# Kernel optimization log

Measured on AMD Instinct MI355X. Metric: run time of the kernel, lower is better.

Reference implementation:

```python
import jax, jax.numpy as jnp
import numpy as np

HEADS = 8
NUM_LANDMARKS = 256
PINV_ITERS = 6
KERNEL = 33
PAD = KERNEL // 2


def moore_penrose_iter_pinv(x, iters=PINV_ITERS):
    abs_x = jnp.abs(x)
    col = abs_x.sum(axis=-1)
    row = abs_x.sum(axis=-2)
    z = jnp.swapaxes(x, -1, -2) / (jnp.max(col) * jnp.max(row))
    I = jnp.eye(x.shape[-1], dtype=x.dtype)
    for _ in range(iters):
        xz = x @ z
        z = 0.25 * z @ (13.0 * I - xz @ (15.0 * I - xz @ (7.0 * I - xz)))
    return z


def setup_inputs() -> dict:
    key = jax.random.key(0)
    k1, k2, k3, k4 = jax.random.split(key, 4)
    b, h, n, d = 2, HEADS, 8192, 64
    q = jax.random.normal(k1, (b, h, n, d), dtype=jnp.float32)
    k = jax.random.normal(k2, (b, h, n, d), dtype=jnp.float32)
    v = jax.random.normal(k3, (b, h, n, d), dtype=jnp.float32)
    conv_w = jax.random.normal(k4, (HEADS, 1, KERNEL, 1), dtype=jnp.float32) * 0.05
    return {"q": q, "k": k, "v": v, "conv_w": conv_w}


def reference(q, k, v, conv_w):
    b, h, n, d = q.shape
    m = NUM_LANDMARKS
    l = n // m  # n chosen divisible by m, so no padding branch

    # landmarks: mean over contiguous groups of size l
    q_land = q.reshape(b, h, m, l, d).sum(axis=-2) / l  # [b,h,m,d]
    k_land = k.reshape(b, h, m, l, d).sum(axis=-2) / l

    sim1 = jnp.einsum('bhid,bhjd->bhij', q, k_land)       # [b,h,n,m]
    sim2 = jnp.einsum('bhid,bhjd->bhij', q_land, k_land)  # [b,h,m,m]
    sim3 = jnp.einsum('bhid,bhjd->bhij', q_land, k)       # [b,h,m,n]

    attn1 = jax.nn.softmax(sim1, axis=-1)
    attn2 = jax.nn.softmax(sim2, axis=-1)
    attn3 = jax.nn.softmax(sim3, axis=-1)

    attn2_inv = moore_penrose_iter_pinv(attn2, PINV_ITERS)

    out = attn1 @ (attn2_inv @ (attn3 @ v))  # [b,h,n,d]

    # depthwise residual conv over sequence dim (Conv2d(h,h,(33,1),groups=h,bias=False) on v)
    res = jax.lax.conv_general_dilated(
        v, conv_w,
        window_strides=(1, 1),
        padding=((PAD, PAD), (0, 0)),
        dimension_numbers=('NCHW', 'OIHW', 'NCHW'),
        feature_group_count=HEADS,
    )
    return out + res
```

## Files before the change

### kernel.cpp

```cpp
#include <hip/hip_runtime.h>


#define N_SEQ 8192
#define NBH   16
#define MLAND 256
#define DHEAD 64
#define NSPLIT3 8
#define MM_E  (NBH * MLAND * MLAND)
#define LM_E  (NBH * MLAND * DHEAD)

typedef __attribute__((ext_vector_type(8))) short bfrag;
typedef __attribute__((ext_vector_type(8))) _Float16 hfrag;
typedef __attribute__((ext_vector_type(4))) float f32x4;

__device__ __forceinline__ void fma8(float (&o)[8], float p, const float4& a, const float4& b) {
    o[0] += p * a.x; o[1] += p * a.y; o[2] += p * a.z; o[3] += p * a.w;
    o[4] += p * b.x; o[5] += p * b.y; o[6] += p * b.z; o[7] += p * b.w;
}

__device__ __forceinline__ float bf2f(unsigned short h) {
    return __uint_as_float(((unsigned)h) << 16);
}

__device__ __forceinline__ void splitbf(float v, unsigned short& h, unsigned short& l) {
    unsigned bits = __float_as_uint(v);
    h = (unsigned short)(bits >> 16);
    float r = v - __uint_as_float(bits & 0xffff0000u);
    l = (unsigned short)(__float_as_uint(r) >> 16);
}

__device__ __forceinline__ void splith(float v, unsigned short& h, unsigned short& l) {
    _Float16 hf = (_Float16)v;
    _Float16 lf = (_Float16)(v - (float)hf);
    h = __builtin_bit_cast(unsigned short, hf);
    l = __builtin_bit_cast(unsigned short, lf);
}

__device__ __forceinline__ void stage16(const float* __restrict__ src,
                                        unsigned short* dh, unsigned short* dl) {
    unsigned* ph = (unsigned*)dh;
    unsigned* pl = (unsigned*)dl;
    #pragma unroll
    for (int o = 0; o < 16; o += 4) {
        float4 a = *(const float4*)(src + o);
        float vv[4] = {a.x, a.y, a.z, a.w};
        unsigned short h[4], l[4];
        #pragma unroll
        for (int u = 0; u < 4; ++u) splitbf(vv[u], h[u], l[u]);
        ph[o / 2]     = (unsigned)h[0] | ((unsigned)h[1] << 16);
        ph[o / 2 + 1] = (unsigned)h[2] | ((unsigned)h[3] << 16);
        pl[o / 2]     = (unsigned)l[0] | ((unsigned)l[1] << 16);
        pl[o / 2 + 1] = (unsigned)l[2] | ((unsigned)l[3] << 16);
    }
}

__device__ __forceinline__ void stageh16(const float* __restrict__ src,
                                         unsigned short* dh, unsigned short* dl) {
    unsigned* ph = (unsigned*)dh;
    unsigned* pl = (unsigned*)dl;
    #pragma unroll
    for (int o = 0; o < 16; o += 4) {
        float4 a = *(const float4*)(src + o);
        float vv[4] = {a.x, a.y, a.z, a.w};
        unsigned short h[4], l[4];
        #pragma unroll
        for (int u = 0; u < 4; ++u) splith(vv[u], h[u], l[u]);
        ph[o / 2]     = (unsigned)h[0] | ((unsigned)h[1] << 16);
        ph[o / 2 + 1] = (unsigned)h[2] | ((unsigned)h[3] << 16);
        pl[o / 2]     = (unsigned)l[0] | ((unsigned)l[1] << 16);
        pl[o / 2 + 1] = (unsigned)l[2] | ((unsigned)l[3] << 16);
    }
}

__global__ __launch_bounds__(64) void k_landmarks(
    const float* __restrict__ q, const float* __restrict__ k,
    float* __restrict__ ql, float* __restrict__ kl)
{
    int mi = blockIdx.x & 255;
    int bh = blockIdx.x >> 8;
    const float* src = blockIdx.y ? k : q;
    float*       dst = blockIdx.y ? kl : ql;
    int t = threadIdx.x;
    const float* s = src + ((size_t)bh * N_SEQ + (size_t)mi * 32) * DHEAD;
    float acc = 0.f;
    #pragma unroll
    for (int j = 0; j < 32; ++j) acc += s[j * DHEAD + t];
    dst[((size_t)bh * MLAND + mi) * DHEAD + t] = acc * (1.f / 32.f);
}

__global__ __launch_bounds__(256) void k_sim2_softmax(
    const float* __restrict__ ql, const float* __restrict__ kl,
    unsigned short* __restrict__ xs)
{
    unsigned short* xh = xs;
    unsigned short* xl = xs + MM_E;
    int bh = blockIdx.x >> 8;
    int i  = blockIdx.x & 255;
    int t  = threadIdx.x;
    __shared__ float qrow[DHEAD];
    __shared__ float wred[8];
    if (t < DHEAD) qrow[t] = ql[((size_t)bh * MLAND + i) * DHEAD + t];
    __syncthreads();
    const float* krow = kl + ((size_t)bh * MLAND + t) * DHEAD;
    float s = 0.f;
    #pragma unroll
    for (int kk = 0; kk < DHEAD; kk += 4) {
        float4 k4 = *(const float4*)(krow + kk);
        s += qrow[kk] * k4.x + qrow[kk + 1] * k4.y + qrow[kk + 2] * k4.z + qrow[kk + 3] * k4.w;
    }
    float m = s;
    #pragma unroll
    for (int o = 32; o > 0; o >>= 1) m = fmaxf(m, __shfl_xor(m, o, 64));
    int wave = t >> 6, lane = t & 63;
    if (lane == 0) wred[wave] = m;
    __syncthreads();
    float bm = fmaxf(fmaxf(wred[0], wred[1]), fmaxf(wred[2], wred[3]));
    float e = __expf(s - bm);
    float sum = e;
    #pragma unroll
    for (int o = 32; o > 0; o >>= 1) sum += __shfl_xor(sum, o, 64);
    if (lane == 0) wred[4 + wave] = sum;
    __syncthreads();
    float bs = wred[4] + wred[5] + wred[6] + wred[7];
    float val = e / bs;
    unsigned short h, l;
    splitbf(val, h, l);
    size_t idx = ((size_t)bh * MLAND + i) * MLAND + t;
    xh[idx] = h;
    xl[idx] = l;
}

__global__ __launch_bounds__(256) void k_scale_reduce(
    const unsigned short* __restrict__ xs, float* __restrict__ scl)
{
    const unsigned short* xh = xs;
    const unsigned short* xl = xs + MM_E;
    int bh = blockIdx.y, seg = blockIdx.x;
    int t = threadIdx.x;
    size_t b = (size_t)bh * MLAND * MLAND;
    __shared__ float red[32];
    __shared__ float red2[256];

    {
        int r = seg * 16 + (t >> 4);
        int j0 = (t & 15) * 16;
        float rp = 0.f;
        #pragma unroll
        for (int j = 0; j < 16; ++j) {
            size_t idx = b + (size_t)r * MLAND + j0 + j;
            rp += bf2f(xh[idx]) + bf2f(xl[idx]);
        }
        rp += __shfl_xor(rp, 1, 16);
        rp += __shfl_xor(rp, 2, 16);
        rp += __shfl_xor(rp, 4, 16);
        rp += __shfl_xor(rp, 8, 16);
        if ((t & 15) == 0) red[t >> 4] = rp;
        __syncthreads();
        if (t == 0) {
            float m = red[0];
            #pragma unroll
            for (int i = 1; i < 16; ++i) m = fmaxf(m, red[i]);
            atomicMax((unsigned int*)&scl[0], __float_as_uint(m));
        }
        __syncthreads();
    }
    {
        int c = seg * 16 + (t & 15);
        int i0 = (t >> 4) * 16;
        float cp = 0.f;
        #pragma unroll
        for (int i = 0; i < 16; ++i) {
            size_t idx = b + (size_t)(i0 + i) * MLAND + c;
            cp += bf2f(xh[idx]) + bf2f(xl[idx]);
        }
        red2[t] = cp;
        __syncthreads();
        if (t < 16) {
            float s = 0.f;
            #pragma unroll
            for (int g = 0; g < 16; ++g) s += red2[g * 16 + t];
            red[t] = s;
        }
        __syncthreads();
        if (t == 0) {
            float m = red[0];
            #pragma unroll
            for (int i = 1; i < 16; ++i) m = fmaxf(m, red[i]);
            atomicMax((unsigned int*)&scl[1], __float_as_uint(m));
        }
    }
}

__global__ __launch_bounds__(256) void k_zinit(
    const unsigned short* __restrict__ xs, unsigned short* __restrict__ zs,
    const float* __restrict__ scl)
{
    const unsigned short* xh = xs;
    const unsigned short* xl = xs + MM_E;
    unsigned short* zh = zs;
    unsigned short* zl = zs + MM_E;
    __shared__ float tile[32][33];
    int bh = blockIdx.z;
    int i0 = blockIdx.y * 32, j0 = blockIdx.x * 32;
    int t = threadIdx.x;
    int lx = t & 31, ly = t >> 5;
    size_t b = (size_t)bh * MLAND * MLAND;
    #pragma unroll
    for (int p = 0; p < 4; ++p) {
        size_t idx = b + (size_t)(i0 + ly + 8 * p) * MLAND + j0 + lx;
        tile[ly + 8 * p][lx] = bf2f(xh[idx]) + bf2f(xl[idx]);
    }
    __syncthreads();
    float inv = 1.0f / (scl[0] * scl[1]);
    #pragma unroll
    for (int p = 0; p < 4; ++p) {
        float val = tile[lx][ly + 8 * p] * inv;
        unsigned short h, l;
        splitbf(val, h, l);
        size_t idx = b + (size_t)(j0 + ly + 8 * p) * MLAND + i0 + lx;
        zh[idx] = h;
        zl[idx] = l;
    }
}

__global__ __launch_bounds__(256) void k_bmm_planes(
    const unsigned short* __restrict__ Ahp, const unsigned short* __restrict__ Alp,
    const unsigned short* __restrict__ Bhp, const unsigned short* __restrict__ Blp,
    unsigned short* __restrict__ Chp, unsigned short* __restrict__ Clp,
    float* __restrict__ Cf,
    int N, float diag, float bscale, float outscale)
{
    __shared__ unsigned short sm[2 * 32 * 72 + 2 * 64 * 72];
    unsigned short* Ah = sm;
    unsigned short* Al = sm + 32 * 72;
    unsigned short* Bh = sm + 2 * 32 * 72;
    unsigned short* Bl = sm + 2 * 32 * 72 + 64 * 72;

    int ntn = N >> 6;
    int bid = blockIdx.x;
    int xcd  = bid & 7;
    int slot = bid >> 3;
    int bh   = xcd + 8 * (slot & 1);
    int tile = slot >> 1;
    int m0 = (tile / ntn) * 32, n0 = (tile % ntn) * 64;

    const size_t abase = (size_t)bh * 65536;
    const size_t bbase = (size_t)bh * 256 * N;
    int t = threadIdx.x;
    int wave = t >> 6, lane = t & 63;
    int l15 = lane & 15, quad = lane >> 4;
    int wr = wave >> 1, wc = wave & 1;
    unsigned sflip = (bscale < 0.f) ? 0x8000u : 0u;

    f32x4 acc[2] = {};

    for (int kc = 0; kc < 256; kc += 64) {
        __syncthreads();
        {
            int m = t & 31, ks = (t >> 5) * 8;
            size_t off = abase + (size_t)(m0 + m) * 256 + kc + ks;
            *(uint4*)&Ah[m * 72 + ks] = *(const uint4*)&Ahp[off];
            *(uint4*)&Al[m * 72 + ks] = *(const uint4*)&Alp[off];
        }
        {
            int kk = t & 63, ns = (t >> 6) * 16;
            int gk = kc + kk;
            size_t off = bbase + (size_t)gk * N + n0 + ns;
            unsigned short hb[16], lb[16];
            *(uint4*)&hb[0] = *(const uint4*)&Bhp[off];
            *(uint4*)&hb[8] = *(const uint4*)&Bhp[off + 8];
            *(uint4*)&lb[0] = *(const uint4*)&Blp[off];
            *(uint4*)&lb[8] = *(const uint4*)&Blp[off + 8];
            #pragma unroll
            for (int u = 0; u < 16; ++u) {
                unsigned short h = hb[u] ^ sflip;
                unsigned short l = lb[u] ^ sflip;
                if (diag != 0.f && gk == n0 + ns + u) {
                    float val = diag + bf2f(h) + bf2f(l);
                    splitbf(val, h, l);
                }
                Bh[(ns + u) * 72 + kk] = h;
                Bl[(ns + u) * 72 + kk] = l;
            }
        }
        __syncthreads();

        #pragma unroll
        for (int k0 = 0; k0 < 64; k0 += 32) {
            int kf = k0 + quad * 8;
            int am = wr * 16 + l15;
            bfrag ah = *(const bfrag*)&Ah[am * 72 + kf];
            bfrag al = *(const bfrag*)&Al[am * 72 + kf];
            #pragma unroll
            for (int j = 0; j < 2; ++j) {
                int bn = wc * 32 + j * 16 + l15;
                bfrag bhf = *(const bfrag*)&Bh[bn * 72 + kf];
                bfrag blf = *(const bfrag*)&Bl[bn * 72 + kf];
                acc[j] = __builtin_amdgcn_mfma_f32_16x16x32_bf16(al, bhf, acc[j], 0, 0, 0);
                acc[j] = __builtin_amdgcn_mfma_f32_16x16x32_bf16(ah, blf, acc[j], 0, 0, 0);
                acc[j] = __builtin_amdgcn_mfma_f32_16x16x32_bf16(ah, bhf, acc[j], 0, 0, 0);
            }
        }
    }

    size_t cbase = (size_t)bh * 256 * N;
    if (Cf) {
        #pragma unroll
        for (int j = 0; j < 2; ++j) {
            #pragma unroll
            for (int r = 0; r < 4; ++r) {
                int row = m0 + wr * 16 + quad * 4 + r;
                int col = n0 + wc * 32 + j * 16 + l15;
                Cf[cbase + (size_t)row * N + col] = acc[j][r] * outscale;
            }
        }
    } else {
        #pragma unroll
        for (int j = 0; j < 2; ++j) {
            #pragma unroll
            for (int r = 0; r < 4; ++r) {
                int row = m0 + wr * 16 + quad * 4 + r;
                int col = n0 + wc * 32 + j * 16 + l15;
                float val = acc[j][r] * outscale;
                unsigned short h, l;
                splitbf(val, h, l);
                size_t idx = cbase + (size_t)row * N + col;
                Chp[idx] = h;
                Clp[idx] = l;
            }
        }
    }
}

__global__ __launch_bounds__(256, 2) void k_attn3_partial(
    const float* __restrict__ ql, const float* __restrict__ k,
    const float* __restrict__ v, float* __restrict__ pO,
    float* __restrict__ pm, float* __restrict__ pl)
{
    __shared__ __align__(16) unsigned short sm3[36864];
    unsigned short* QH = sm3;
    unsigned short* QL = sm3 + 4608;
    unsigned short* KH = sm3 + 9216;
    unsigned short* KL = sm3 + 13824;
    unsigned short* VH = sm3 + 18432;
    unsigned short* VL = sm3 + 23040;
    unsigned short* PH = sm3 + 27648;
    unsigned short* PL = sm3 + 32256;

    int sp = blockIdx.x;
    int m0 = blockIdx.y * 64;
    int bh = blockIdx.z;
    int t = threadIdx.x;
    int wave = t >> 6, lane = t & 63;
    int l15 = lane & 15, quad = lane >> 4;

    {
        int row = t & 63, ds = (t >> 6) * 16;
        const float* src = ql + ((size_t)bh * MLAND + m0 + row) * DHEAD + ds;
        stage16(src, &QH[row * 72 + ds], &QL[row * 72 + ds]);
    }
    __syncthreads();

    bfrag aqh[2], aql[2];
    #pragma unroll
    for (int ks = 0; ks < 2; ++ks) {
        aqh[ks] = *(const bfrag*)&QH[(wave * 16 + l15) * 72 + ks * 32 + quad * 8];
        aql[ks] = *(const bfrag*)&QL[(wave * 16 + l15) * 72 + ks * 32 + quad * 8];
    }

    f32x4 O[4] = {};
    float M[4], L[4];
    #pragma unroll
    for (int r = 0; r < 4; ++r) { M[r] = -1e30f; L[r] = 0.f; }

    const float* kb = k + (size_t)bh * N_SEQ * DHEAD;
    const float* vb = v + (size_t)bh * N_SEQ * DHEAD;

    for (int cc = 0; cc < 16; ++cc) {
        int c0 = sp * 1024 + cc * 64;
        __syncthreads();
        {
            int key = t & 63, ds = (t >> 6) * 16;
            stage16(kb + (size_t)(c0 + key) * DHEAD + ds,
                    &KH[key * 72 + ds], &KL[key * 72 + ds]);
        }
        {
            int key = t & 63, dq = (t >> 6) * 16;
            const float* src = vb + (size_t)(c0 + key) * DHEAD + dq;
            #pragma unroll
            for (int o = 0; o < 16; o += 4) {
                float4 a = *(const float4*)(src + o);
                float vv[4] = {a.x, a.y, a.z, a.w};
                #pragma unroll
                for (int u = 0; u < 4; ++u) {
                    unsigned short h, l;
                    splitbf(vv[u], h, l);
                    VH[(dq + o + u) * 72 + key] = h;
                    VL[(dq + o + u) * 72 + key] = l;
                }
            }
        }
        __syncthreads();

        f32x4 S4[4] = {};
        __builtin_amdgcn_s_setprio(1);
        #pragma unroll
        for (int ks = 0; ks < 2; ++ks) {
            #pragma unroll
            for (int ni = 0; ni < 4; ++ni) {
                bfrag bkh = *(const bfrag*)&KH[(ni * 16 + l15) * 72 + ks * 32 + quad * 8];
                bfrag bkl = *(const bfrag*)&KL[(ni * 16 + l15) * 72 + ks * 32 + quad * 8];
                S4[ni] = __builtin_amdgcn_mfma_f32_16x16x32_bf16(aql[ks], bkh, S4[ni], 0, 0, 0);
                S4[ni] = __builtin_amdgcn_mfma_f32_16x16x32_bf16(aqh[ks], bkl, S4[ni], 0, 0, 0);
                S4[ni] = __builtin_amdgcn_mfma_f32_16x16x32_bf16(aqh[ks], bkh, S4[ni], 0, 0, 0);
            }
        }
        __builtin_amdgcn_s_setprio(0);

        #pragma unroll
        for (int r = 0; r < 4; ++r) {
            float mv = fmaxf(fmaxf(S4[0][r], S4[1][r]), fmaxf(S4[2][r], S4[3][r]));
            mv = fmaxf(mv, __shfl_xor(mv, 1, 16));
            mv = fmaxf(mv, __shfl_xor(mv, 2, 16));
            mv = fmaxf(mv, __shfl_xor(mv, 4, 16));
            mv = fmaxf(mv, __shfl_xor(mv, 8, 16));
            float nM = fmaxf(M[r], mv);
            float alpha = __expf(M[r] - nM);
            M[r] = nM;
            float rs = 0.f;
            #pragma unroll
            for (int ni = 0; ni < 4; ++ni) {
                float p = __expf(S4[ni][r] - nM);
                S4[ni][r] = p;
                rs += p;
            }
            rs += __shfl_xor(rs, 1, 16);
            rs += __shfl_xor(rs, 2, 16);
            rs += __shfl_xor(rs, 4, 16);
            rs += __shfl_xor(rs, 8, 16);
            L[r] = L[r] * alpha + rs;
            #pragma unroll
            for (int ni = 0; ni < 4; ++ni) O[ni][r] *= alpha;
        }

        #pragma unroll
        for (int ni = 0; ni < 4; ++ni) {
            #pragma unroll
            for (int r = 0; r < 4; ++r) {
                int row = wave * 16 + quad * 4 + r;
                int col = ni * 16 + l15;
                unsigned short h, l;
                splitbf(S4[ni][r], h, l);
                PH[row * 72 + col] = h;
                PL[row * 72 + col] = l;
            }
        }

        __builtin_amdgcn_s_setprio(1);
        #pragma unroll
        for (int ks = 0; ks < 2; ++ks) {
            bfrag aph = *(const bfrag*)&PH[(wave * 16 + l15) * 72 + ks * 32 + quad * 8];
            bfrag apl = *(const bfrag*)&PL[(wave * 16 + l15) * 72 + ks * 32 + quad * 8];
            #pragma unroll
            for (int ni = 0; ni < 4; ++ni) {
                bfrag bvh = *(const bfrag*)&VH[(ni * 16 + l15) * 72 + ks * 32 + quad * 8];
                bfrag bvl = *(const bfrag*)&VL[(ni * 16 + l15) * 72 + ks * 32 + quad * 8];
                O[ni] = __builtin_amdgcn_mfma_f32_16x16x32_bf16(apl, bvh, O[ni], 0, 0, 0);
                O[ni] = __builtin_amdgcn_mfma_f32_16x16x32_bf16(aph, bvl, O[ni], 0, 0, 0);
                O[ni] = __builtin_amdgcn_mfma_f32_16x16x32_bf16(aph, bvh, O[ni], 0, 0, 0);
            }
        }
        __builtin_amdgcn_s_setprio(0);
    }

    int base = (bh * NSPLIT3 + sp) * MLAND + m0;
    #pragma unroll
    for (int r = 0; r < 4; ++r) {
        int row = wave * 16 + quad * 4 + r;
        if (l15 == 0) { pm[base + row] = M[r]; pl[base + row] = L[r]; }
        #pragma unroll
        for (int ni = 0; ni < 4; ++ni)
            pO[(size_t)(base + row) * DHEAD + ni * 16 + l15] = O[ni][r];
    }
}

__global__ __launch_bounds__(64) void k_attn3_combine(
    const float* __restrict__ pO, const float* __restrict__ pm,
    const float* __restrict__ pl, unsigned short* __restrict__ kvs)
{
    unsigned short* kvh = kvs;
    unsigned short* kvl = kvs + LM_E;
    int bh = blockIdx.x >> 8;
    int m  = blockIdx.x & 255;
    int d  = threadIdx.x;
    float M = -1e30f;
    #pragma unroll
    for (int s = 0; s < NSPLIT3; ++s) M = fmaxf(M, pm[(bh * NSPLIT3 + s) * MLAND + m]);
    float L = 0.f, O = 0.f;
    #pragma unroll
    for (int s = 0; s < NSPLIT3; ++s) {
        int base = (bh * NSPLIT3 + s) * MLAND + m;
        float w = __expf(pm[base] - M);
        L += pl[base] * w;
        O += w * pO[(size_t)base * DHEAD + d];
    }
    float val = O / L;
    unsigned short h, l;
    splitbf(val, h, l);
    size_t idx = ((size_t)bh * MLAND + m) * DHEAD + d;
    kvh[idx] = h;
    kvl[idx] = l;
}

__global__ __launch_bounds__(256, 2) void k_attn1_mfma(
    const float* __restrict__ q, const float* __restrict__ kl,
    const float* __restrict__ W, float* __restrict__ out)
{
    __shared__ __align__(16) unsigned short sm1[36864];
    unsigned short* QH = sm1;
    unsigned short* QL = sm1 + 4608;
    unsigned short* KH = sm1 + 9216;
    unsigned short* KL = sm1 + 13824;
    unsigned short* WH = sm1 + 18432;
    unsigned short* WL = sm1 + 23040;
    unsigned short* PH = sm1 + 27648;
    unsigned short* PL = sm1 + 32256;

    int bh = blockIdx.y;
    int r0 = blockIdx.x * 64;
    int t = threadIdx.x;
    int wave = t >> 6, lane = t & 63;
    int l15 = lane & 15, quad = lane >> 4;

    {
        int row = t & 63, ds = (t >> 6) * 16;
        const float* src = q + ((size_t)bh * N_SEQ + r0 + row) * DHEAD + ds;
        stageh16(src, &QH[row * 72 + ds], &QL[row * 72 + ds]);
    }
    __syncthreads();

    hfrag aqh[2], aql[2];
    #pragma unroll
    for (int ks = 0; ks < 2; ++ks) {
        aqh[ks] = *(const hfrag*)&QH[(wave * 16 + l15) * 72 + ks * 32 + quad * 8];
        aql[ks] = *(const hfrag*)&QL[(wave * 16 + l15) * 72 + ks * 32 + quad * 8];
    }

    f32x4 O4[4] = {};
    float M[4], L[4];
    #pragma unroll
    for (int r = 0; r < 4; ++r) { M[r] = -1e30f; L[r] = 0.f; }

    for (int mc = 0; mc < 4; ++mc) {
        __syncthreads();
        {
            int key = t & 63, ds = (t >> 6) * 16;
            stageh16(kl + ((size_t)bh * MLAND + mc * 64 + key) * DHEAD + ds,
                     &KH[key * 72 + ds], &KL[key * 72 + ds]);
        }
        {
            int key = t & 63, dq = (t >> 6) * 16;
            const float* src = W + ((size_t)bh * MLAND + mc * 64 + key) * DHEAD + dq;
            #pragma unroll
            for (int o = 0; o < 16; o += 4) {
                float4 a = *(const float4*)(src + o);
                float vv[4] = {a.x * 0.015625f, a.y * 0.015625f,
                               a.z * 0.015625f, a.w * 0.015625f};
                #pragma unroll
                for (int u = 0; u < 4; ++u) {
                    unsigned short h, l;
                    splith(vv[u], h, l);
                    WH[(dq + o + u) * 72 + key] = h;
                    WL[(dq + o + u) * 72 + key] = l;
                }
            }
        }
        __syncthreads();

        f32x4 S4[4] = {};
        __builtin_amdgcn_s_setprio(1);
        #pragma unroll
        for (int ks = 0; ks < 2; ++ks) {
            #pragma unroll
            for (int ni = 0; ni < 4; ++ni) {
                hfrag bkh = *(const hfrag*)&KH[(ni * 16 + l15) * 72 + ks * 32 + quad * 8];
                hfrag bkl = *(const hfrag*)&KL[(ni * 16 + l15) * 72 + ks * 32 + quad * 8];
                S4[ni] = __builtin_amdgcn_mfma_f32_16x16x32_f16(aql[ks], bkh, S4[ni], 0, 0, 0);
                S4[ni] = __builtin_amdgcn_mfma_f32_16x16x32_f16(aqh[ks], bkl, S4[ni], 0, 0, 0);
                S4[ni] = __builtin_amdgcn_mfma_f32_16x16x32_f16(aqh[ks], bkh, S4[ni], 0, 0, 0);
            }
        }
        __builtin_amdgcn_s_setprio(0);

        #pragma unroll
        for (int r = 0; r < 4; ++r) {
            float mv = fmaxf(fmaxf(S4[0][r], S4[1][r]), fmaxf(S4[2][r], S4[3][r]));
            mv = fmaxf(mv, __shfl_xor(mv, 1, 16));
            mv = fmaxf(mv, __shfl_xor(mv, 2, 16));
            mv = fmaxf(mv, __shfl_xor(mv, 4, 16));
            mv = fmaxf(mv, __shfl_xor(mv, 8, 16));
            float nM = fmaxf(M[r], mv);
            float alpha = __expf(M[r] - nM);
            M[r] = nM;
            float rs = 0.f;
            #pragma unroll
            for (int ni = 0; ni < 4; ++ni) {
                float p = __expf(S4[ni][r] - nM);
                S4[ni][r] = p;
                rs += p;
            }
            rs += __shfl_xor(rs, 1, 16);
            rs += __shfl_xor(rs, 2, 16);
            rs += __shfl_xor(rs, 4, 16);
            rs += __shfl_xor(rs, 8, 16);
            L[r] = L[r] * alpha + rs;
            #pragma unroll
            for (int ni = 0; ni < 4; ++ni) O4[ni][r] *= alpha;
        }

        #pragma unroll
        for (int ni = 0; ni < 4; ++ni) {
            #pragma unroll
            for (int r = 0; r < 4; ++r) {
                int row = wave * 16 + quad * 4 + r;
                int col = ni * 16 + l15;
                unsigned short h, l;
                splith(S4[ni][r], h, l);
                PH[row * 72 + col] = h;
                PL[row * 72 + col] = l;
            }
        }

        __builtin_amdgcn_s_setprio(1);
        #pragma unroll
        for (int ks = 0; ks < 2; ++ks) {
            hfrag aph = *(const hfrag*)&PH[(wave * 16 + l15) * 72 + ks * 32 + quad * 8];
            hfrag apl = *(const hfrag*)&PL[(wave * 16 + l15) * 72 + ks * 32 + quad * 8];
            #pragma unroll
            for (int ni = 0; ni < 4; ++ni) {
                hfrag bwh = *(const hfrag*)&WH[(ni * 16 + l15) * 72 + ks * 32 + quad * 8];
                hfrag bwl = *(const hfrag*)&WL[(ni * 16 + l15) * 72 + ks * 32 + quad * 8];
                O4[ni] = __builtin_amdgcn_mfma_f32_16x16x32_f16(apl, bwh, O4[ni], 0, 0, 0);
                O4[ni] = __builtin_amdgcn_mfma_f32_16x16x32_f16(aph, bwl, O4[ni], 0, 0, 0);
                O4[ni] = __builtin_amdgcn_mfma_f32_16x16x32_f16(aph, bwh, O4[ni], 0, 0, 0);
            }
        }
        __builtin_amdgcn_s_setprio(0);
    }

    float inv[4];
    #pragma unroll
    for (int r = 0; r < 4; ++r) inv[r] = 64.0f / L[r];
    #pragma unroll
    for (int r = 0; r < 4; ++r) {
        int row = wave * 16 + quad * 4 + r;
        float* dst = out + ((size_t)bh * N_SEQ + r0 + row) * DHEAD;
        #pragma unroll
        for (int ni = 0; ni < 4; ++ni)
            dst[ni * 16 + l15] = O4[ni][r] * inv[r];
    }
}

__global__ __launch_bounds__(256) void k_conv_add(
    const float* __restrict__ v, const float* __restrict__ cw,
    float* __restrict__ out)
{
    __shared__ __align__(16) float smem[160 * 68];
    __shared__ float wgt[33];
    int bh = blockIdx.y;
    int r0 = blockIdx.x * 128;
    int t = threadIdx.x;
    int wave = t >> 6, lane = t & 63;
    int ly = lane >> 3, lx = lane & 7;
    int rb = wave * 32 + ly * 4;

    if (t < 33) wgt[t] = cw[(bh & 7) * 33 + t];

    for (int rr = t; rr < 160; rr += 256) {
        int gr = r0 - 16 + rr;
        bool ok = (gr >= 0) && (gr < N_SEQ);
        const float* src = v + ((size_t)bh * N_SEQ + gr) * DHEAD;
        #pragma unroll
        for (int c = 0; c < 64; c += 4) {
            float4 val = ok ? *(const float4*)(src + c) : make_float4(0.f, 0.f, 0.f, 0.f);
            *(float4*)&smem[rr * 68 + c] = val;
        }
    }
    __syncthreads();

    float res[4][8] = {};
    #pragma unroll
    for (int w = 0; w < 36; ++w) {
        float4 va  = *(const float4*)&smem[(rb + w) * 68 + lx * 8];
        float4 vb4 = *(const float4*)&smem[(rb + w) * 68 + lx * 8 + 4];
        #pragma unroll
        for (int i = 0; i < 4; ++i) {
            if (w - i >= 0 && w - i <= 32) {
                float wv = wgt[w - i];
                fma8(res[i], wv, va, vb4);
            }
        }
    }

    #pragma unroll
    for (int i = 0; i < 4; ++i) {
        float* dst = out + ((size_t)bh * N_SEQ + r0 + rb + i) * DHEAD + lx * 8;
        float4 o0 = *(const float4*)dst;
        float4 o1 = *(const float4*)(dst + 4);
        *(float4*)dst = make_float4(o0.x + res[i][0], o0.y + res[i][1],
                                    o0.z + res[i][2], o0.w + res[i][3]);
        *(float4*)(dst + 4) = make_float4(o1.x + res[i][4], o1.y + res[i][5],
                                          o1.z + res[i][6], o1.w + res[i][7]);
    }
}

extern "C" void kernel_launch(void* const* d_in, const int* in_sizes, int n_in,
                              void* d_out, int out_size, void* d_ws, size_t ws_size,
                              hipStream_t stream)
{
    (void)in_sizes; (void)n_in; (void)out_size; (void)ws_size;
    const float* q  = (const float*)d_in[0];
    const float* k  = (const float*)d_in[1];
    const float* v  = (const float*)d_in[2];
    const float* cw = (const float*)d_in[3];
    float* out = (float*)d_out;
    float* ws  = (float*)d_ws;

    const size_t LM = (size_t)LM_E;
    const size_t MM = (size_t)MM_E;

    float* ql  = ws;
    float* kl  = ql  + LM;
    float* xsf = kl  + LM;
    float* zsf = xsf + MM;
    float* big = zsf + MM;
    float* kvf = big + 4 * MM;
    float* W   = kvf + LM;
    float* scl = W   + LM;
    float* pm  = scl + 16;
    float* pl  = pm + (size_t)NBH * NSPLIT3 * MLAND;

    float* pO = big;

    unsigned short* xs  = (unsigned short*)xsf;
    unsigned short* zs  = (unsigned short*)zsf;
    unsigned short* bgu = (unsigned short*)big;
    unsigned short* kvs = (unsigned short*)kvf;

    unsigned short* xh  = xs;
    unsigned short* xl  = xs + MM;
    unsigned short* zh  = zs;
    unsigned short* zl  = zs + MM;
    unsigned short* z2h = bgu;
    unsigned short* z2l = bgu + MM;
    unsigned short* xzh = bgu + 2 * MM;
    unsigned short* xzl = bgu + 3 * MM;
    unsigned short* t2h = bgu + 4 * MM;
    unsigned short* t2l = bgu + 5 * MM;
    unsigned short* t3h = bgu + 6 * MM;
    unsigned short* t3l = bgu + 7 * MM;
    unsigned short* kvh = kvs;
    unsigned short* kvl = kvs + LM;

    hipMemsetAsync(scl, 0, 32, stream);

    k_landmarks<<<dim3(NBH * MLAND, 2), 64, 0, stream>>>(q, k, ql, kl);
    k_sim2_softmax<<<NBH * MLAND, 256, 0, stream>>>(ql, kl, xs);
    k_scale_reduce<<<dim3(16, NBH), 256, 0, stream>>>(xs, scl);
    k_zinit<<<dim3(8, 8, NBH), 256, 0, stream>>>(xs, zs, scl);

    k_attn3_partial<<<dim3(NSPLIT3, 4, NBH), 256, 0, stream>>>(ql, k, v, pO, pm, pl);
    k_attn3_combine<<<NBH * MLAND, 64, 0, stream>>>(pO, pm, pl, kvs);

    unsigned short *zch = zh, *zcl = zl, *znh = z2h, *znl = z2l;
    for (int it = 0; it < 6; ++it) {
        k_bmm_planes<<<512, 256, 0, stream>>>(
            xh, xl, zch, zcl, xzh, xzl, nullptr, 256, 0.f, 1.f, 1.f);
        k_bmm_planes<<<512, 256, 0, stream>>>(
            xzh, xzl, xzh, xzl, t2h, t2l, nullptr, 256, 7.f, -1.f, 1.f);
        k_bmm_planes<<<512, 256, 0, stream>>>(
            xzh, xzl, t2h, t2l, t3h, t3l, nullptr, 256, 15.f, -1.f, 1.f);
        k_bmm_planes<<<512, 256, 0, stream>>>(
            zch, zcl, t3h, t3l, znh, znl, nullptr, 256, 13.f, -1.f, 0.25f);
        unsigned short* th = zch; zch = znh; znh = th;
        unsigned short* tl = zcl; zcl = znl; znl = tl;
    }
    k_bmm_planes<<<128, 256, 0, stream>>>(
        zch, zcl, kvh, kvl, nullptr, nullptr, W, 64, 0.f, 1.f, 1.f);

    k_attn1_mfma<<<dim3(128, NBH), 256, 0, stream>>>(q, kl, W, out);
    k_conv_add<<<dim3(64, NBH), 256, 0, stream>>>(v, cw, out);
}
```

Baseline: 568.1 us.

## Widen k-chunk to 128 and prefetch second half into registers in bmm_planes

Replaces the four-iteration k-loop (64-wide chunks) in the split-bf16 batched matmul with two 128-wide chunks. The global loads for the second chunk are issued into registers before the first chunk's MFMAs run, overlapping memory latency with compute and halving the number of barrier pairs. The shared-memory footprint roughly doubles and register pressure grows, which may reduce occupancy.

```diff
diff --git a/kernel.cpp b/kernel.cpp
--- a/kernel.cpp
+++ b/kernel.cpp
@@ -230,11 +230,11 @@
     float* __restrict__ Cf,
     int N, float diag, float bscale, float outscale)
 {
-    __shared__ unsigned short sm[2 * 32 * 72 + 2 * 64 * 72];
+    __shared__ __align__(16) unsigned short sm[26112];
     unsigned short* Ah = sm;
-    unsigned short* Al = sm + 32 * 72;
-    unsigned short* Bh = sm + 2 * 32 * 72;
-    unsigned short* Bl = sm + 2 * 32 * 72 + 64 * 72;
+    unsigned short* Al = sm + 4352;
+    unsigned short* Bh = sm + 8704;
+    unsigned short* Bl = sm + 17408;
 
     int ntn = N >> 6;
     int bid = blockIdx.x;
@@ -252,54 +252,110 @@
     int wr = wave >> 1, wc = wave & 1;
     unsigned sflip = (bscale < 0.f) ? 0x8000u : 0u;
 
+    int am_ = t & 31, aks = (t >> 5) * 16;
+    int bkk = t & 127, bns = (t >> 7) * 32;
+
     f32x4 acc[2] = {};
-
-    for (int kc = 0; kc < 256; kc += 64) {
-        __syncthreads();
-        {
-            int m = t & 31, ks = (t >> 5) * 8;
-            size_t off = abase + (size_t)(m0 + m) * 256 + kc + ks;
-            *(uint4*)&Ah[m * 72 + ks] = *(const uint4*)&Ahp[off];
-            *(uint4*)&Al[m * 72 + ks] = *(const uint4*)&Alp[off];
-        }
-        {
-            int kk = t & 63, ns = (t >> 6) * 16;
-            int gk = kc + kk;
-            size_t off = bbase + (size_t)gk * N + n0 + ns;
-            unsigned short hb[16], lb[16];
-            *(uint4*)&hb[0] = *(const uint4*)&Bhp[off];
-            *(uint4*)&hb[8] = *(const uint4*)&Bhp[off + 8];
-            *(uint4*)&lb[0] = *(const uint4*)&Blp[off];
-            *(uint4*)&lb[8] = *(const uint4*)&Blp[off + 8];
-            #pragma unroll
-            for (int u = 0; u < 16; ++u) {
-                unsigned short h = hb[u] ^ sflip;
-                unsigned short l = lb[u] ^ sflip;
-                if (diag != 0.f && gk == n0 + ns + u) {
-                    float val = diag + bf2f(h) + bf2f(l);
-                    splitbf(val, h, l);
-                }
-                Bh[(ns + u) * 72 + kk] = h;
-                Bl[(ns + u) * 72 + kk] = l;
-            }
-        }
-        __syncthreads();
-
-        #pragma unroll
-        for (int k0 = 0; k0 < 64; k0 += 32) {
-            int kf = k0 + quad * 8;
-            int am = wr * 16 + l15;
-            bfrag ah = *(const bfrag*)&Ah[am * 72 + kf];
-            bfrag al = *(const bfrag*)&Al[am * 72 + kf];
-            #pragma unroll
-            for (int j = 0; j < 2; ++j) {
-                int bn = wc * 32 + j * 16 + l15;
-                bfrag bhf = *(const bfrag*)&Bh[bn * 72 + kf];
-                bfrag blf = *(const bfrag*)&Bl[bn * 72 + kf];
-                acc[j] = __builtin_amdgcn_mfma_f32_16x16x32_bf16(al, bhf, acc[j], 0, 0, 0);
-                acc[j] = __builtin_amdgcn_mfma_f32_16x16x32_bf16(ah, blf, acc[j], 0, 0, 0);
-                acc[j] = __builtin_amdgcn_mfma_f32_16x16x32_bf16(ah, bhf, acc[j], 0, 0, 0);
-            }
+    uint4 rah0, rah1, ral0, ral1;
+    uint4 rbh0, rbh1, rbh2, rbh3, rbl0, rbl1, rbl2, rbl3;
+
+    {
+        size_t offA = abase + (size_t)(m0 + am_) * 256 + aks;
+        rah0 = *(const uint4*)&Ahp[offA];      rah1 = *(const uint4*)&Ahp[offA + 8];
+        ral0 = *(const uint4*)&Alp[offA];      ral1 = *(const uint4*)&Alp[offA + 8];
+        size_t offB = bbase + (size_t)bkk * N + n0 + bns;
+        rbh0 = *(const uint4*)&Bhp[offB];      rbh1 = *(const uint4*)&Bhp[offB + 8];
+        rbh2 = *(const uint4*)&Bhp[offB + 16]; rbh3 = *(const uint4*)&Bhp[offB + 24];
+        rbl0 = *(const uint4*)&Blp[offB];      rbl1 = *(const uint4*)&Blp[offB + 8];
+        rbl2 = *(const uint4*)&Blp[offB + 16]; rbl3 = *(const uint4*)&Blp[offB + 24];
+    }
+    {
+        unsigned short* da = &Ah[am_ * 136 + aks];
+        *(uint4*)da = rah0; *(uint4*)(da + 8) = rah1;
+        unsigned short* dl2 = &Al[am_ * 136 + aks];
+        *(uint4*)dl2 = ral0; *(uint4*)(dl2 + 8) = ral1;
+        unsigned short hb[32], lb[32];
+        *(uint4*)&hb[0] = rbh0;  *(uint4*)&hb[8] = rbh1;
+        *(uint4*)&hb[16] = rbh2; *(uint4*)&hb[24] = rbh3;
+        *(uint4*)&lb[0] = rbl0;  *(uint4*)&lb[8] = rbl1;
+        *(uint4*)&lb[16] = rbl2; *(uint4*)&lb[24] = rbl3;
+        int gk = bkk;
+        #pragma unroll
+        for (int u = 0; u < 32; ++u) {
+            unsigned short h = hb[u] ^ sflip;
+            unsigned short l = lb[u] ^ sflip;
+            if (diag != 0.f && gk == n0 + bns + u) {
+                float val = diag + bf2f(h) + bf2f(l);
+                splitbf(val, h, l);
+            }
+            Bh[(bns + u) * 136 + bkk] = h;
+            Bl[(bns + u) * 136 + bkk] = l;
+        }
+    }
+    {
+        size_t offA = abase + (size_t)(m0 + am_) * 256 + 128 + aks;
+        rah0 = *(const uint4*)&Ahp[offA];      rah1 = *(const uint4*)&Ahp[offA + 8];
+        ral0 = *(const uint4*)&Alp[offA];      ral1 = *(const uint4*)&Alp[offA + 8];
+        size_t offB = bbase + (size_t)(128 + bkk) * N + n0 + bns;
+        rbh0 = *(const uint4*)&Bhp[offB];      rbh1 = *(const uint4*)&Bhp[offB + 8];
+        rbh2 = *(const uint4*)&Bhp[offB + 16]; rbh3 = *(const uint4*)&Bhp[offB + 24];
+        rbl0 = *(const uint4*)&Blp[offB];      rbl1 = *(const uint4*)&Blp[offB + 8];
+        rbl2 = *(const uint4*)&Blp[offB + 16]; rbl3 = *(const uint4*)&Blp[offB + 24];
+    }
+    __syncthreads();
+    #pragma unroll
+    for (int k0 = 0; k0 < 128; k0 += 32) {
+        int kf = k0 + quad * 8;
+        bfrag ah = *(const bfrag*)&Ah[(wr * 16 + l15) * 136 + kf];
+        bfrag al = *(const bfrag*)&Al[(wr * 16 + l15) * 136 + kf];
+        #pragma unroll
+        for (int j = 0; j < 2; ++j) {
+            int bn = wc * 32 + j * 16 + l15;
+            bfrag bhf = *(const bfrag*)&Bh[bn * 136 + kf];
+            bfrag blf = *(const bfrag*)&Bl[bn * 136 + kf];
+            acc[j] = __builtin_amdgcn_mfma_f32_16x16x32_bf16(al, bhf, acc[j], 0, 0, 0);
+            acc[j] = __builtin_amdgcn_mfma_f32_16x16x32_bf16(ah, blf, acc[j], 0, 0, 0);
+            acc[j] = __builtin_amdgcn_mfma_f32_16x16x32_bf16(ah, bhf, acc[j], 0, 0, 0);
+        }
+    }
+    __syncthreads();
+    {
+        unsigned short* da = &Ah[am_ * 136 + aks];
+        *(uint4*)da = rah0; *(uint4*)(da + 8) = rah1;
+        unsigned short* dl2 = &Al[am_ * 136 + aks];
+        *(uint4*)dl2 = ral0; *(uint4*)(dl2 + 8) = ral1;
+        unsigned short hb[32], lb[32];
+        *(uint4*)&hb[0] = rbh0;  *(uint4*)&hb[8] = rbh1;
+        *(uint4*)&hb[16] = rbh2; *(uint4*)&hb[24] = rbh3;
+        *(uint4*)&lb[0] = rbl0;  *(uint4*)&lb[8] = rbl1;
+        *(uint4*)&lb[16] = rbl2; *(uint4*)&lb[24] = rbl3;
+        int gk = 128 + bkk;
+        #pragma unroll
+        for (int u = 0; u < 32; ++u) {
+            unsigned short h = hb[u] ^ sflip;
+            unsigned short l = lb[u] ^ sflip;
+            if (diag != 0.f && gk == n0 + bns + u) {
+                float val = diag + bf2f(h) + bf2f(l);
+                splitbf(val, h, l);
+            }
+            Bh[(bns + u) * 136 + bkk] = h;
+            Bl[(bns + u) * 136 + bkk] = l;
+        }
+    }
+    __syncthreads();
+    #pragma unroll
+    for (int k0 = 0; k0 < 128; k0 += 32) {
+        int kf = k0 + quad * 8;
+        bfrag ah = *(const bfrag*)&Ah[(wr * 16 + l15) * 136 + kf];
+        bfrag al = *(const bfrag*)&Al[(wr * 16 + l15) * 136 + kf];
+        #pragma unroll
+        for (int j = 0; j < 2; ++j) {
+            int bn = wc * 32 + j * 16 + l15;
+            bfrag bhf = *(const bfrag*)&Bh[bn * 136 + kf];
+            bfrag blf = *(const bfrag*)&Bl[bn * 136 + kf];
+            acc[j] = __builtin_amdgcn_mfma_f32_16x16x32_bf16(al, bhf, acc[j], 0, 0, 0);
+            acc[j] = __builtin_amdgcn_mfma_f32_16x16x32_bf16(ah, blf, acc[j], 0, 0, 0);
+            acc[j] = __builtin_amdgcn_mfma_f32_16x16x32_bf16(ah, bhf, acc[j], 0, 0, 0);
         }
     }
 
```

Result: no change. 571.7 us (+0.6%).

## Expand pinv Newton step polynomial into parallel GEMMs with fp32 z accumulation

Applied to the files above, without the earlier changes.

The Moore-Penrose iteration is rewritten algebraically as z_new = 3.25z - 3.75zY + 1.75zY^2 - 0.25(zY)Y^2 with Y = xz. This lets independent GEMMs run as two roles inside one launch, cutting the dependent chain from four launches to three per iteration. The polynomial terms are accumulated into an fp32 z buffer via atomics, and z is split into bf16 hi/lo planes on the fly when staged into shared memory. This costs one extra GEMM per iteration, float atomics and an in-kernel conversion, in exchange for a shorter critical path and fewer launches.

```diff
diff --git a/kernel.cpp b/kernel.cpp
--- a/kernel.cpp
+++ b/kernel.cpp
@@ -192,13 +192,11 @@
 }
 
 __global__ __launch_bounds__(256) void k_zinit(
-    const unsigned short* __restrict__ xs, unsigned short* __restrict__ zs,
+    const unsigned short* __restrict__ xs, float* __restrict__ zf,
     const float* __restrict__ scl)
 {
     const unsigned short* xh = xs;
     const unsigned short* xl = xs + MM_E;
-    unsigned short* zh = zs;
-    unsigned short* zl = zs + MM_E;
     __shared__ float tile[32][33];
     int bh = blockIdx.z;
     int i0 = blockIdx.y * 32, j0 = blockIdx.x * 32;
@@ -215,72 +213,87 @@
     #pragma unroll
     for (int p = 0; p < 4; ++p) {
         float val = tile[lx][ly + 8 * p] * inv;
-        unsigned short h, l;
-        splitbf(val, h, l);
         size_t idx = b + (size_t)(j0 + ly + 8 * p) * MLAND + i0 + lx;
-        zh[idx] = h;
-        zl[idx] = l;
-    }
-}
-
-__global__ __launch_bounds__(256) void k_bmm_planes(
+        zf[idx] = val;
+    }
+}
+
+__device__ __forceinline__ void gemm_tile(
+    unsigned short* sm,
     const unsigned short* __restrict__ Ahp, const unsigned short* __restrict__ Alp,
+    const float* __restrict__ Afp,
     const unsigned short* __restrict__ Bhp, const unsigned short* __restrict__ Blp,
-    unsigned short* __restrict__ Chp, unsigned short* __restrict__ Clp,
-    float* __restrict__ Cf,
-    int N, float diag, float bscale, float outscale)
-{
-    __shared__ unsigned short sm[2 * 32 * 72 + 2 * 64 * 72];
+    const float* __restrict__ Bfp,
+    int N, int bh, int m0, int n0, int t, f32x4* acc)
+{
     unsigned short* Ah = sm;
     unsigned short* Al = sm + 32 * 72;
     unsigned short* Bh = sm + 2 * 32 * 72;
     unsigned short* Bl = sm + 2 * 32 * 72 + 64 * 72;
 
-    int ntn = N >> 6;
-    int bid = blockIdx.x;
-    int xcd  = bid & 7;
-    int slot = bid >> 3;
-    int bh   = xcd + 8 * (slot & 1);
-    int tile = slot >> 1;
-    int m0 = (tile / ntn) * 32, n0 = (tile % ntn) * 64;
-
     const size_t abase = (size_t)bh * 65536;
     const size_t bbase = (size_t)bh * 256 * N;
-    int t = threadIdx.x;
     int wave = t >> 6, lane = t & 63;
     int l15 = lane & 15, quad = lane >> 4;
     int wr = wave >> 1, wc = wave & 1;
-    unsigned sflip = (bscale < 0.f) ? 0x8000u : 0u;
-
-    f32x4 acc[2] = {};
 
     for (int kc = 0; kc < 256; kc += 64) {
         __syncthreads();
         {
             int m = t & 31, ks = (t >> 5) * 8;
-            size_t off = abase + (size_t)(m0 + m) * 256 + kc + ks;
-            *(uint4*)&Ah[m * 72 + ks] = *(const uint4*)&Ahp[off];
-            *(uint4*)&Al[m * 72 + ks] = *(const uint4*)&Alp[off];
+            if (Afp) {
+                const float* src = Afp + abase + (size_t)(m0 + m) * 256 + kc + ks;
+                uint4 hv, lv;
+                float4 a0 = *(const float4*)(src);
+                float4 a1 = *(const float4*)(src + 4);
+                unsigned short h[8], l[8];
+                float vv[8] = {a0.x, a0.y, a0.z, a0.w, a1.x, a1.y, a1.z, a1.w};
+                #pragma unroll
+                for (int u = 0; u < 8; ++u) splitbf(vv[u], h[u], l[u]);
+                hv.x = (unsigned)h[0] | ((unsigned)h[1] << 16);
+                hv.y = (unsigned)h[2] | ((unsigned)h[3] << 16);
+                hv.z = (unsigned)h[4] | ((unsigned)h[5] << 16);
+                hv.w = (unsigned)h[6] | ((unsigned)h[7] << 16);
+                lv.x = (unsigned)l[0] | ((unsigned)l[1] << 16);
+                lv.y = (unsigned)l[2] | ((unsigned)l[3] << 16);
+                lv.z = (unsigned)l[4] | ((unsigned)l[5] << 16);
+                lv.w = (unsigned)l[6] | ((unsigned)l[7] << 16);
+                *(uint4*)&Ah[m * 72 + ks] = hv;
+                *(uint4*)&Al[m * 72 + ks] = lv;
+            } else {
+                size_t off = abase + (size_t)(m0 + m) * 256 + kc + ks;
+                *(uint4*)&Ah[m * 72 + ks] = *(const uint4*)&Ahp[off];
+                *(uint4*)&Al[m * 72 + ks] = *(const uint4*)&Alp[off];
+            }
         }
         {
             int kk = t & 63, ns = (t >> 6) * 16;
-            int gk = kc + kk;
-            size_t off = bbase + (size_t)gk * N + n0 + ns;
-            unsigned short hb[16], lb[16];
-            *(uint4*)&hb[0] = *(const uint4*)&Bhp[off];
-            *(uint4*)&hb[8] = *(const uint4*)&Bhp[off + 8];
-            *(uint4*)&lb[0] = *(const uint4*)&Blp[off];
-            *(uint4*)&lb[8] = *(const uint4*)&Blp[off + 8];
-            #pragma unroll
-            for (int u = 0; u < 16; ++u) {
-                unsigned short h = hb[u] ^ sflip;
-                unsigned short l = lb[u] ^ sflip;
-                if (diag != 0.f && gk == n0 + ns + u) {
-                    float val = diag + bf2f(h) + bf2f(l);
-                    splitbf(val, h, l);
+            if (Bfp) {
+                const float* src = Bfp + bbase + (size_t)(kc + kk) * N + n0 + ns;
+                #pragma unroll
+                for (int o = 0; o < 16; o += 4) {
+                    float4 a = *(const float4*)(src + o);
+                    float vv[4] = {a.x, a.y, a.z, a.w};
+                    #pragma unroll
+                    for (int u = 0; u < 4; ++u) {
+                        unsigned short h, l;
+                        splitbf(vv[u], h, l);
+                        Bh[(ns + o + u) * 72 + kk] = h;
+                        Bl[(ns + o + u) * 72 + kk] = l;
+                    }
                 }
-                Bh[(ns + u) * 72 + kk] = h;
-                Bl[(ns + u) * 72 + kk] = l;
+            } else {
+                size_t off = bbase + (size_t)(kc + kk) * N + n0 + ns;
+                unsigned short hb[16], lb[16];
+                *(uint4*)&hb[0] = *(const uint4*)&Bhp[off];
+                *(uint4*)&hb[8] = *(const uint4*)&Bhp[off + 8];
+                *(uint4*)&lb[0] = *(const uint4*)&Blp[off];
+                *(uint4*)&lb[8] = *(const uint4*)&Blp[off + 8];
+                #pragma unroll
+                for (int u = 0; u < 16; ++u) {
+                    Bh[(ns + u) * 72 + kk] = hb[u];
+                    Bl[(ns + u) * 72 + kk] = lb[u];
+                }
             }
         }
         __syncthreads();
@@ -302,34 +315,163 @@
             }
         }
     }
-
-    size_t cbase = (size_t)bh * 256 * N;
-    if (Cf) {
-        #pragma unroll
-        for (int j = 0; j < 2; ++j) {
+}
+
+__global__ __launch_bounds__(256) void k_gemm_y(
+    const unsigned short* __restrict__ xh, const unsigned short* __restrict__ xl,
+    const float* __restrict__ zcf,
+    unsigned short* __restrict__ yh, unsigned short* __restrict__ yl)
+{
+    __shared__ __align__(16) unsigned short sm[13824];
+    int bid = blockIdx.x;
+    int xcd = bid & 7, slot = bid >> 3;
+    int bh = xcd + 8 * (slot & 1);
+    int tile = slot >> 1;
+    int m0 = (tile >> 2) * 32, n0 = (tile & 3) * 64;
+    int t = threadIdx.x;
+    f32x4 acc[2] = {};
+    gemm_tile(sm, xh, xl, nullptr, nullptr, nullptr, zcf, 256, bh, m0, n0, t, acc);
+
+    int wave = t >> 6, lane = t & 63, l15 = lane & 15, quad = lane >> 4;
+    int wr = wave >> 1, wc = wave & 1;
+    size_t cb = (size_t)bh * 65536;
+    #pragma unroll
+    for (int j = 0; j < 2; ++j)
+        #pragma unroll
+        for (int r = 0; r < 4; ++r) {
+            int row = m0 + wr * 16 + quad * 4 + r;
+            int col = n0 + wc * 32 + j * 16 + l15;
+            unsigned short h, l;
+            splitbf(acc[j][r], h, l);
+            size_t idx = cb + (size_t)row * 256 + col;
+            yh[idx] = h;
+            yl[idx] = l;
+        }
+}
+
+__global__ __launch_bounds__(256) void k_gemm_l2(
+    const unsigned short* __restrict__ yh, const unsigned short* __restrict__ yl,
+    const float* __restrict__ zcf,
+    unsigned short* __restrict__ y2h, unsigned short* __restrict__ y2l,
+    unsigned short* __restrict__ w1h, unsigned short* __restrict__ w1l,
+    float* __restrict__ znf)
+{
+    __shared__ __align__(16) unsigned short sm[13824];
+    int bid = blockIdx.x;
+    int xcd = bid & 7, s = bid >> 3;
+    int role = s & 1, s2 = s >> 1;
+    int bh = xcd + 8 * (s2 & 1);
+    int tile = s2 >> 1;
+    int m0 = (tile >> 2) * 32, n0 = (tile & 3) * 64;
+    int t = threadIdx.x;
+    f32x4 acc[2] = {};
+
+    int wave = t >> 6, lane = t & 63, l15 = lane & 15, quad = lane >> 4;
+    int wr = wave >> 1, wc = wave & 1;
+    size_t cb = (size_t)bh * 65536;
+
+    if (role == 0) {
+        gemm_tile(sm, yh, yl, nullptr, yh, yl, nullptr, 256, bh, m0, n0, t, acc);
+        #pragma unroll
+        for (int j = 0; j < 2; ++j)
             #pragma unroll
             for (int r = 0; r < 4; ++r) {
                 int row = m0 + wr * 16 + quad * 4 + r;
                 int col = n0 + wc * 32 + j * 16 + l15;
-                Cf[cbase + (size_t)row * N + col] = acc[j][r] * outscale;
-            }
-        }
+                unsigned short h, l;
+                splitbf(acc[j][r], h, l);
+                size_t idx = cb + (size_t)row * 256 + col;
+                y2h[idx] = h;
+                y2l[idx] = l;
+            }
     } else {
-        #pragma unroll
-        for (int j = 0; j < 2; ++j) {
+        gemm_tile(sm, nullptr, nullptr, zcf, yh, yl, nullptr, 256, bh, m0, n0, t, acc);
+        #pragma unroll
+        for (int j = 0; j < 2; ++j)
             #pragma unroll
             for (int r = 0; r < 4; ++r) {
                 int row = m0 + wr * 16 + quad * 4 + r;
                 int col = n0 + wc * 32 + j * 16 + l15;
-                float val = acc[j][r] * outscale;
+                float w1v = acc[j][r];
                 unsigned short h, l;
-                splitbf(val, h, l);
-                size_t idx = cbase + (size_t)row * N + col;
-                Chp[idx] = h;
-                Clp[idx] = l;
-            }
-        }
-    }
+                splitbf(w1v, h, l);
+                size_t idx = cb + (size_t)row * 256 + col;
+                w1h[idx] = h;
+                w1l[idx] = l;
+                znf[idx] = 3.25f * zcf[idx] - 3.75f * w1v;
+            }
+    }
+}
+
+__global__ __launch_bounds__(256) void k_gemm_l3(
+    const float* __restrict__ zcf,
+    const unsigned short* __restrict__ y2h, const unsigned short* __restrict__ y2l,
+    const unsigned short* __restrict__ w1h, const unsigned short* __restrict__ w1l,
+    float* __restrict__ znf)
+{
+    __shared__ __align__(16) unsigned short sm[13824];
+    int bid = blockIdx.x;
+    int xcd = bid & 7, s = bid >> 3;
+    int role = s & 1, s2 = s >> 1;
+    int bh = xcd + 8 * (s2 & 1);
+    int tile = s2 >> 1;
+    int m0 = (tile >> 2) * 32, n0 = (tile & 3) * 64;
+    int t = threadIdx.x;
+    f32x4 acc[2] = {};
+
+    int wave = t >> 6, lane = t & 63, l15 = lane & 15, quad = lane >> 4;
+    int wr = wave >> 1, wc = wave & 1;
+    size_t cb = (size_t)bh * 65536;
+
+    if (role == 0) {
+        gemm_tile(sm, nullptr, nullptr, zcf, y2h, y2l, nullptr, 256, bh, m0, n0, t, acc);
+        #pragma unroll
+        for (int j = 0; j < 2; ++j)
+            #pragma unroll
+            for (int r = 0; r < 4; ++r) {
+                int row = m0 + wr * 16 + quad * 4 + r;
+                int col = n0 + wc * 32 + j * 16 + l15;
+                atomicAdd(&znf[cb + (size_t)row * 256 + col], 1.75f * acc[j][r]);
+            }
+    } else {
+        gemm_tile(sm, w1h, w1l, nullptr, y2h, y2l, nullptr, 256, bh, m0, n0, t, acc);
+        #pragma unroll
+        for (int j = 0; j < 2; ++j)
+            #pragma unroll
+            for (int r = 0; r < 4; ++r) {
+                int row = m0 + wr * 16 + quad * 4 + r;
+                int col = n0 + wc * 32 + j * 16 + l15;
+                atomicAdd(&znf[cb + (size_t)row * 256 + col], -0.25f * acc[j][r]);
+            }
+    }
+}
+
+__global__ __launch_bounds__(256) void k_gemm_w(
+    const float* __restrict__ zf,
+    const unsigned short* __restrict__ kvh, const unsigned short* __restrict__ kvl,
+    float* __restrict__ W)
+{
+    __shared__ __align__(16) unsigned short sm[13824];
+    int bid = blockIdx.x;
+    int xcd = bid & 7, slot = bid >> 3;
+    int bh = xcd + 8 * (slot & 1);
+    int tile = slot >> 1;
+    int m0 = tile * 32, n0 = 0;
+    int t = threadIdx.x;
+    f32x4 acc[2] = {};
+    gemm_tile(sm, nullptr, nullptr, zf, kvh, kvl, nullptr, 64, bh, m0, n0, t, acc);
+
+    int wave = t >> 6, lane = t & 63, l15 = lane & 15, quad = lane >> 4;
+    int wr = wave >> 1, wc = wave & 1;
+    size_t cb = (size_t)bh * 256 * 64;
+    #pragma unroll
+    for (int j = 0; j < 2; ++j)
+        #pragma unroll
+        for (int r = 0; r < 4; ++r) {
+            int row = m0 + wr * 16 + quad * 4 + r;
+            int col = wc * 32 + j * 16 + l15;
+            W[cb + (size_t)row * 64 + col] = acc[j][r];
+        }
 }
 
 __global__ __launch_bounds__(256, 2) void k_attn3_partial(
@@ -732,61 +874,50 @@
     float* ql  = ws;
     float* kl  = ql  + LM;
     float* xsf = kl  + LM;
-    float* zsf = xsf + MM;
-    float* big = zsf + MM;
+    float* zf0 = xsf + MM;
+    float* big = zf0 + MM;
     float* kvf = big + 4 * MM;
     float* W   = kvf + LM;
     float* scl = W   + LM;
     float* pm  = scl + 16;
     float* pl  = pm + (size_t)NBH * NSPLIT3 * MLAND;
 
-    float* pO = big;
+    float* pO  = big;
+    float* zf1 = big;
 
     unsigned short* xs  = (unsigned short*)xsf;
-    unsigned short* zs  = (unsigned short*)zsf;
-    unsigned short* bgu = (unsigned short*)big;
     unsigned short* kvs = (unsigned short*)kvf;
 
     unsigned short* xh  = xs;
-    unsigned short* xl  = xs + MM;
-    unsigned short* zh  = zs;
-    unsigned short* zl  = zs + MM;
-    unsigned short* z2h = bgu;
-    unsigned short* z2l = bgu + MM;
-    unsigned short* xzh = bgu + 2 * MM;
-    unsigned short* xzl = bgu + 3 * MM;
-    unsigned short* t2h = bgu + 4 * MM;
-    unsigned short* t2l = bgu + 5 * MM;
-    unsigned short* t3h = bgu + 6 * MM;
-    unsigned short* t3l = bgu + 7 * MM;
+    unsigned short* xl  = xs + MM_E;
+    unsigned short* yh  = (unsigned short*)(big + MM);
+    unsigned short* yl  = yh + MM_E;
+    unsigned short* y2h = (unsigned short*)(big + 2 * MM);
+    unsigned short* y2l = y2h + MM_E;
+    unsigned short* w1h = (unsigned short*)(big + 3 * MM);
+    unsigned short* w1l = w1h + MM_E;
     unsigned short* kvh = kvs;
-    unsigned short* kvl = kvs + LM;
+    unsigned short* kvl = kvs + LM_E;
 
     hipMemsetAsync(scl, 0, 32, stream);
 
     k_landmarks<<<dim3(NBH * MLAND, 2), 64, 0, stream>>>(q, k, ql, kl);
     k_sim2_softmax<<<NBH * MLAND, 256, 0, stream>>>(ql, kl, xs);
     k_scale_reduce<<<dim3(16, NBH), 256, 0, stream>>>(xs, scl);
-    k_zinit<<<dim3(8, 8, NBH), 256, 0, stream>>>(xs, zs, scl);
+    k_zinit<<<dim3(8, 8, NBH), 256, 0, stream>>>(xs, zf0, scl);
 
     k_attn3_partial<<<dim3(NSPLIT3, 4, NBH), 256, 0, stream>>>(ql, k, v, pO, pm, pl);
     k_attn3_combine<<<NBH * MLAND, 64, 0, stream>>>(pO, pm, pl, kvs);
 
-    unsigned short *zch = zh, *zcl = zl, *znh = z2h, *znl = z2l;
+    float* zc = zf0;
+    float* zn = zf1;
     for (int it = 0; it < 6; ++it) {
-        k_bmm_planes<<<512, 256, 0, stream>>>(
-            xh, xl, zch, zcl, xzh, xzl, nullptr, 256, 0.f, 1.f, 1.f);
-        k_bmm_planes<<<512, 256, 0, stream>>>(
-            xzh, xzl, xzh, xzl, t2h, t2l, nullptr, 256, 7.f, -1.f, 1.f);
-        k_bmm_planes<<<512, 256, 0, stream>>>(
-            xzh, xzl, t2h, t2l, t3h, t3l, nullptr, 256, 15.f, -1.f, 1.f);
-        k_bmm_planes<<<512, 256, 0, stream>>>(
-            zch, zcl, t3h, t3l, znh, znl, nullptr, 256, 13.f, -1.f, 0.25f);
-        unsigned short* th = zch; zch = znh; znh = th;
-        unsigned short* tl = zcl; zcl = znl; znl = tl;
-    }
-    k_bmm_planes<<<128, 256, 0, stream>>>(
-        zch, zcl, kvh, kvl, nullptr, nullptr, W, 64, 0.f, 1.f, 1.f);
+        k_gemm_y<<<512, 256, 0, stream>>>(xh, xl, zc, yh, yl);
+        k_gemm_l2<<<1024, 256, 0, stream>>>(yh, yl, zc, y2h, y2l, w1h, w1l, zn);
+        k_gemm_l3<<<1024, 256, 0, stream>>>(zc, y2h, y2l, w1h, w1l, zn);
+        float* tt = zc; zc = zn; zn = tt;
+    }
+    k_gemm_w<<<128, 256, 0, stream>>>(zc, kvh, kvl, W);
 
     k_attn1_mfma<<<dim3(128, NBH), 256, 0, stream>>>(q, kl, W, out);
     k_conv_add<<<dim3(64, NBH), 256, 0, stream>>>(v, cw, out);
```

After: 580.9 us. +2.3%, slower.
